# Kernel optimization log

Hardware: AMD Instinct MI355X
Metric: run time of the kernel (lower is better)

Reference implementation:

```python
import math
import jax, jax.numpy as jnp
import numpy as np

HEADS = 16


def setup_inputs() -> dict:
    key = jax.random.key(0)
    k1, k2, k3 = jax.random.split(key, 3)
    bs, n_ctx, width = 2, 2048, 1024
    x = jax.random.normal(k1, (bs, n_ctx, width), dtype=jnp.float32)
    # init_scale=0.25 style small init for stability
    W_qkv = jax.random.normal(k2, (width, 3 * width), dtype=jnp.float32) * (0.25 / math.sqrt(width))
    b_qkv = jnp.zeros((3 * width,), dtype=jnp.float32)
    W_proj = jax.random.normal(k3, (width, width), dtype=jnp.float32) * (0.25 / math.sqrt(width))
    b_proj = jnp.zeros((width,), dtype=jnp.float32)
    return {"x": x, "W_qkv": W_qkv, "b_qkv": b_qkv, "W_proj": W_proj, "b_proj": b_proj}


def reference(x, W_qkv, b_qkv, W_proj, b_proj):
    bs, n_ctx, width = x.shape
    qkv = x @ W_qkv + b_qkv                     # [b, s, 3*width]
    attn_ch = width // HEADS                    # head dim
    qkv = qkv.reshape(bs, n_ctx, HEADS, 3 * attn_ch)
    q, k, v = jnp.split(qkv, 3, axis=-1)        # each [b, s, h, c]
    scale = 1.0 / math.sqrt(math.sqrt(attn_ch)) # applied to both q and k
    weight = jnp.einsum('bthc,bshc->bhts', q * scale, k * scale)
    weight = jax.nn.softmax(weight.astype(jnp.float32), axis=-1).astype(qkv.dtype)
    out = jnp.einsum('bhts,bshc->bthc', weight, v).reshape(bs, n_ctx, width)
    return out @ W_proj + b_proj
```

## Files before the change

kernel.cpp:

```cpp
#include <hip/hip_runtime.h>


using u16 = unsigned short;
typedef __attribute__((ext_vector_type(8))) short s16x8;
typedef __attribute__((ext_vector_type(4))) float f32x4;
typedef __attribute__((ext_vector_type(16))) float f32x16;

__device__ __forceinline__ u16 f2bf(float f) {
    unsigned x = __builtin_bit_cast(unsigned, f);
    x += 0x7fffu + ((x >> 16) & 1u);
    return (u16)(x >> 16);
}
__device__ __forceinline__ float bf2f(u16 u) {
    return __builtin_bit_cast(float, ((unsigned)u) << 16);
}
__device__ __forceinline__ unsigned pk2bf(float lo, float hi) {
    unsigned a = __builtin_bit_cast(unsigned, lo);
    unsigned b = __builtin_bit_cast(unsigned, hi);
    a += 0x7fffu + ((a >> 16) & 1u);
    b += 0x7fffu + ((b >> 16) & 1u);
    return (a >> 16) | (b & 0xffff0000u);
}
__device__ __forceinline__ void gll16(const void* g, void* l) {
    __builtin_amdgcn_global_load_lds(
        (const __attribute__((address_space(1))) unsigned int*)g,
        (__attribute__((address_space(3))) unsigned int*)l, 16, 0, 0);
}

#define MFMA(a, b, c)   __builtin_amdgcn_mfma_f32_16x16x32_bf16((a), (b), (c), 0, 0, 0)
#define MFMA32(a, b, c) __builtin_amdgcn_mfma_f32_32x32x16_bf16((a), (b), (c), 0, 0, 0)


__global__ __launch_bounds__(256) void convert_split(const float* __restrict__ in,
                                                     u16* __restrict__ H, u16* __restrict__ L, int n) {
    int i = (blockIdx.x * 256 + threadIdx.x) * 4;
    if (i >= n) return;
    float4 v = *(const float4*)(in + i);
    u16 h0 = f2bf(v.x), h1 = f2bf(v.y), h2 = f2bf(v.z), h3 = f2bf(v.w);
    ushort4 hh = { h0, h1, h2, h3 };
    ushort4 ll = { f2bf(v.x - bf2f(h0)), f2bf(v.y - bf2f(h1)), f2bf(v.z - bf2f(h2)), f2bf(v.w - bf2f(h3)) };
    *(ushort4*)(H + i) = hh;
    *(ushort4*)(L + i) = ll;
}

__global__ __launch_bounds__(256) void transpose_split(const float* __restrict__ W,
                                                       u16* __restrict__ TH, u16* __restrict__ TL,
                                                       int K, int N) {
    __shared__ float st[32][33];
    int n0 = blockIdx.x * 32, k0 = blockIdx.y * 32;
    int c = threadIdx.x & 31, r8 = threadIdx.x >> 5;
#pragma unroll
    for (int i = 0; i < 4; ++i) {
        int r = r8 + i * 8;
        st[r][c] = W[(size_t)(k0 + r) * N + n0 + c];
    }
    __syncthreads();
#pragma unroll
    for (int i = 0; i < 4; ++i) {
        int r = r8 + i * 8;
        float v = st[c][r];
        u16 h = f2bf(v);
        TH[(size_t)(n0 + r) * K + k0 + c] = h;
        TL[(size_t)(n0 + r) * K + k0 + c] = f2bf(v - bf2f(h));
    }
}


template <int EPI>
__global__ __launch_bounds__(256, 2) void gemm_bf16x3(
    const u16* __restrict__ AH, const u16* __restrict__ AL,
    const u16* __restrict__ BTH, const u16* __restrict__ BTL,
    const float* __restrict__ bias,
    u16* __restrict__ Qs, u16* __restrict__ Kb, u16* __restrict__ Vp,
    float* __restrict__ Out) {
    __shared__ u16 sP[2][32][512];

    int id = blockIdx.x;
    int xcd = id & 7, local = id >> 3;
    int nPerX = gridDim.x >> 8;
    int nb = xcd * nPerX + (local >> 5);
    int mb = local & 31;
    int m0 = mb * 128, n0 = nb * 128;

    int tid = threadIdx.x, lane = tid & 63, wv = tid >> 6;
    int g = lane >> 4, c16 = lane & 15;
    int wm = wv >> 1, wn = wv & 1;
    const int lo8 = lane * 8;

    const u16* src[8];
#pragma unroll
    for (int i = 0; i < 8; ++i) {
        int p = wv * 8 + i;
        const u16* arr = (p < 8) ? AH : (p < 16) ? AL : (p < 24) ? BTH : BTL;
        int row0 = ((p < 16) ? m0 : n0) + (p & 7) * 16;
        src[i] = arr + (size_t)(row0 + c16) * 1024 + g * 8;
    }

    f32x4 acc[4][4] = {};

#pragma unroll
    for (int i = 0; i < 8; ++i) gll16(src[i], &sP[0][wv * 8 + i][0]);

    for (int kt = 0; kt < 32; ++kt) {
        int cur = kt & 1;
        __syncthreads();
        if (kt < 31) {
            int ko = (kt + 1) * 32;
#pragma unroll
            for (int i = 0; i < 8; ++i) gll16(src[i] + ko, &sP[cur ^ 1][wv * 8 + i][0]);
        }

        s16x8 ah[4], al[4], bh[4], bl[4];
#pragma unroll
        for (int mi = 0; mi < 4; ++mi) {
            ah[mi] = *(const s16x8*)&sP[cur][wm * 4 + mi][lo8];
            al[mi] = *(const s16x8*)&sP[cur][8 + wm * 4 + mi][lo8];
        }
#pragma unroll
        for (int ni = 0; ni < 4; ++ni) {
            bh[ni] = *(const s16x8*)&sP[cur][16 + wn * 4 + ni][lo8];
            bl[ni] = *(const s16x8*)&sP[cur][24 + wn * 4 + ni][lo8];
        }
#pragma unroll
        for (int mi = 0; mi < 4; ++mi)
#pragma unroll
            for (int ni = 0; ni < 4; ++ni) {
                f32x4 c = acc[mi][ni];
                c = MFMA(ah[mi], bh[ni], c);
                c = MFMA(al[mi], bh[ni], c);
                c = MFMA(ah[mi], bl[ni], c);
                acc[mi][ni] = c;
            }
    }

#pragma unroll
    for (int ni = 0; ni < 4; ++ni) {
        int col = n0 + wn * 64 + ni * 16 + c16;
        float bs = bias[col];
        if (EPI == 0) {
            int h = col / 192;
            int rm = col - h * 192;
#pragma unroll
            for (int mi = 0; mi < 4; ++mi)
#pragma unroll
                for (int r = 0; r < 4; ++r) {
                    int row = m0 + wm * 64 + mi * 16 + 4 * g + r;
                    int b = row >> 11, s = row & 2047;
                    int bh16 = b * 16 + h;
                    float val = acc[mi][ni][r] + bs;
                    if (rm < 64)
                        Qs[(((size_t)bh16 * 2048 + s) << 6) + rm] = f2bf(val * 0.18033688011112042f);
                    else if (rm < 128)
                        Kb[(((size_t)bh16 * 2048 + s) << 6) + rm - 64] = f2bf(val);
                    else {
                        int d = rm - 128;
                        int kg = s >> 4, k16 = s & 15;
                        int mm = (k16 & 3) | (((k16 >> 3) & 1) << 2) | (((k16 >> 2) & 1) << 3);
                        Vp[(((size_t)bh16 * 128 + kg) * 64 + d) * 16 + mm] = f2bf(val);
                    }
                }
        } else {
#pragma unroll
            for (int mi = 0; mi < 4; ++mi)
#pragma unroll
                for (int r = 0; r < 4; ++r) {
                    int row = m0 + wm * 64 + mi * 16 + 4 * g + r;
                    Out[(size_t)row * 1024 + col] = acc[mi][ni][r] + bs;
                }
        }
    }
}

__global__ __launch_bounds__(256, 2) void attn_fwd(
    const u16* __restrict__ Qs, const u16* __restrict__ Kb, const u16* __restrict__ Vp,
    u16* __restrict__ OH, u16* __restrict__ OL) {
    __shared__ u16 sKV[2][16][512];

    int id = blockIdx.x;
    int xcd = id & 7, li = id >> 3;
    int bh = xcd * 4 + (li >> 4);
    int qblk = li & 15;
    int tid = threadIdx.x, w = tid >> 6, lane = tid & 63;
    int l31 = lane & 31, h = lane >> 5;
    int q0 = (qblk * 4 + w) * 32;

    size_t base = (size_t)bh * 2048 * 64;
    size_t vbase = (size_t)bh * 131072;

    const u16* qp = Qs + base + (size_t)(q0 + l31) * 64 + 8 * h;
    s16x8 qf[4];
#pragma unroll
    for (int c = 0; c < 4; ++c) qf[c] = *(const s16x8*)(qp + 16 * c);

    const int pk0 = 2 * w, pk1 = 2 * w + 1;
    const u16* gk0 = Kb + base + (size_t)((pk0 >> 2) * 32 + l31) * 64 + 16 * (pk0 & 3) + 8 * h;
    const u16* gk1 = Kb + base + (size_t)((pk1 >> 2) * 32 + l31) * 64 + 16 * (pk1 & 3) + 8 * h;
    const u16* gv0 = Vp + vbase + (size_t)pk0 * 512 + (size_t)l31 * 16 + 8 * h;
    const u16* gv1 = Vp + vbase + (size_t)pk1 * 512 + (size_t)l31 * 16 + 8 * h;

    auto stage = [&](int buf, int jj) {
        size_t ko = (size_t)jj * 4096;
        gll16(gk0 + ko, &sKV[buf][pk0][0]);
        gll16(gk1 + ko, &sKV[buf][pk1][0]);
        gll16(gv0 + ko, &sKV[buf][8 + pk0][0]);
        gll16(gv1 + ko, &sKV[buf][8 + pk1][0]);
    };

    f32x16 o0 = {}, o1 = {};
    float m = -1e30f, ls = 0.f;
    const int lo = lane * 8;

    stage(0, 0);

    for (int jj = 0; jj < 32; ++jj) {
        int cur = jj & 1;
        __syncthreads();
        if (jj < 31) stage(cur ^ 1, jj + 1);

        s16x8 kf[8], vf[8];
#pragma unroll
        for (int i = 0; i < 8; ++i) {
            kf[i] = *(const s16x8*)&sKV[cur][i][lo];
            vf[i] = *(const s16x8*)&sKV[cur][8 + i][lo];
        }

        f32x16 s0 = {}, s1 = {};
        __builtin_amdgcn_s_setprio(1);
        s0 = MFMA32(kf[0], qf[0], s0);
        s0 = MFMA32(kf[1], qf[1], s0);
        s0 = MFMA32(kf[2], qf[2], s0);
        s0 = MFMA32(kf[3], qf[3], s0);
        s1 = MFMA32(kf[4], qf[0], s1);
        s1 = MFMA32(kf[5], qf[1], s1);
        s1 = MFMA32(kf[6], qf[2], s1);
        s1 = MFMA32(kf[7], qf[3], s1);
        __builtin_amdgcn_s_setprio(0);

        float t0 = fmaxf(s0[0], s1[0]), t1 = fmaxf(s0[1], s1[1]);
        float t2 = fmaxf(s0[2], s1[2]), t3 = fmaxf(s0[3], s1[3]);
#pragma unroll
        for (int r = 4; r < 16; r += 4) {
            t0 = fmaxf(t0, fmaxf(s0[r], s1[r]));
            t1 = fmaxf(t1, fmaxf(s0[r + 1], s1[r + 1]));
            t2 = fmaxf(t2, fmaxf(s0[r + 2], s1[r + 2]));
            t3 = fmaxf(t3, fmaxf(s0[r + 3], s1[r + 3]));
        }
        float pmax = fmaxf(fmaxf(t0, t1), fmaxf(t2, t3));
        pmax = fmaxf(pmax, __shfl_xor(pmax, 32));

        if (!__all(pmax <= m + 8.f)) {
            float mn = fmaxf(m, pmax);
            float f = __builtin_amdgcn_exp2f(m - mn);
            m = mn;
            ls *= f;
#pragma unroll
            for (int r = 0; r < 16; ++r) {
                float fb = __shfl(f, (r & 3) + 8 * (r >> 2) + 4 * h);
                o0[r] *= fb;
                o1[r] *= fb;
            }
        }

        float a0 = 0.f, a1 = 0.f, a2 = 0.f, a3 = 0.f;
#pragma unroll
        for (int r = 0; r < 16; r += 4) {
            s0[r]     = __builtin_amdgcn_exp2f(s0[r] - m);     a0 += s0[r];
            s0[r + 1] = __builtin_amdgcn_exp2f(s0[r + 1] - m); a1 += s0[r + 1];
            s0[r + 2] = __builtin_amdgcn_exp2f(s0[r + 2] - m); a2 += s0[r + 2];
            s0[r + 3] = __builtin_amdgcn_exp2f(s0[r + 3] - m); a3 += s0[r + 3];
            s1[r]     = __builtin_amdgcn_exp2f(s1[r] - m);     a0 += s1[r];
            s1[r + 1] = __builtin_amdgcn_exp2f(s1[r + 1] - m); a1 += s1[r + 1];
            s1[r + 2] = __builtin_amdgcn_exp2f(s1[r + 2] - m); a2 += s1[r + 2];
            s1[r + 3] = __builtin_amdgcn_exp2f(s1[r + 3] - m); a3 += s1[r + 3];
        }
        float sm = (a0 + a1) + (a2 + a3);
        sm += __shfl_xor(sm, 32);
        ls += sm;

        union { s16x8 v8; unsigned u[4]; } p00, p01, p10, p11;
#pragma unroll
        for (int k = 0; k < 4; ++k) {
            p00.u[k] = pk2bf(s0[2 * k], s0[2 * k + 1]);
            p01.u[k] = pk2bf(s0[8 + 2 * k], s0[9 + 2 * k]);
            p10.u[k] = pk2bf(s1[2 * k], s1[2 * k + 1]);
            p11.u[k] = pk2bf(s1[8 + 2 * k], s1[9 + 2 * k]);
        }

        __builtin_amdgcn_s_setprio(1);
        o0 = MFMA32(p00.v8, vf[0], o0);
        o1 = MFMA32(p00.v8, vf[1], o1);
        o0 = MFMA32(p01.v8, vf[2], o0);
        o1 = MFMA32(p01.v8, vf[3], o1);
        o0 = MFMA32(p10.v8, vf[4], o0);
        o1 = MFMA32(p10.v8, vf[5], o1);
        o0 = MFMA32(p11.v8, vf[6], o0);
        o1 = MFMA32(p11.v8, vf[7], o1);
        __builtin_amdgcn_s_setprio(0);
    }

    int b = bh >> 4, hh = bh & 15;
    float inv = 1.0f / ls;
#pragma unroll
    for (int r = 0; r < 16; ++r) {
        int cr = (r & 3) + 8 * (r >> 2) + 4 * h;
        float fb = __shfl(inv, cr);
        int row = q0 + cr;
        size_t idx = ((size_t)(b * 2048 + row)) * 1024 + hh * 64 + l31;
        float v0 = o0[r] * fb, v1 = o1[r] * fb;
        u16 h0 = f2bf(v0);
        OH[idx] = h0;
        OL[idx] = f2bf(v0 - bf2f(h0));
        u16 h1 = f2bf(v1);
        OH[idx + 32] = h1;
        OL[idx + 32] = f2bf(v1 - bf2f(h1));
    }
}


extern "C" void kernel_launch(void* const* d_in, const int* in_sizes, int n_in,
                              void* d_out, int out_size, void* d_ws, size_t ws_size,
                              hipStream_t stream) {
    const float* x     = (const float*)d_in[0];
    const float* Wqkv  = (const float*)d_in[1];
    const float* bqkv  = (const float*)d_in[2];
    const float* Wproj = (const float*)d_in[3];
    const float* bproj = (const float*)d_in[4];
    float* out = (float*)d_out;

    char* w = (char*)d_ws;
    const size_t SZ_X  = (size_t)4096 * 1024 * 2;
    const size_t SZ_WQ = (size_t)3072 * 1024 * 2;
    const size_t SZ_WP = (size_t)1024 * 1024 * 2;
    u16* XH  = (u16*)w; w += SZ_X;
    u16* XL  = (u16*)w; w += SZ_X;
    u16* WQH = (u16*)w; w += SZ_WQ;
    u16* WQL = (u16*)w; w += SZ_WQ;
    u16* WPH = (u16*)w; w += SZ_WP;
    u16* WPL = (u16*)w; w += SZ_WP;
    u16* Q_s = (u16*)w; w += SZ_X;
    u16* K_b = (u16*)w; w += SZ_X;
    u16* V_p = (u16*)w; w += SZ_X;
    u16* OHp = (u16*)w; w += SZ_X;
    u16* OLp = (u16*)w; w += SZ_X;

    convert_split<<<4096, 256, 0, stream>>>(x, XH, XL, 4096 * 1024);
    transpose_split<<<dim3(96, 32), 256, 0, stream>>>(Wqkv, WQH, WQL, 1024, 3072);
    transpose_split<<<dim3(32, 32), 256, 0, stream>>>(Wproj, WPH, WPL, 1024, 1024);
    gemm_bf16x3<0><<<768, 256, 0, stream>>>(XH, XL, WQH, WQL, bqkv, Q_s, K_b, V_p, nullptr);
    attn_fwd<<<512, 256, 0, stream>>>(Q_s, K_b, V_p, OHp, OLp);
    gemm_bf16x3<1><<<256, 256, 0, stream>>>(OHp, OLp, WPH, WPL, bproj, nullptr, nullptr, nullptr, out);
}
```

Measured before the change: 216.9 us.

## Single-buffer GEMM LDS, raise occupancy, drop XCD swizzle, add MFMA priority

```diff
diff --git a/kernel.cpp b/kernel.cpp
--- a/kernel.cpp
+++ b/kernel.cpp
@@ -67,21 +67,15 @@
 
 
 template <int EPI>
-__global__ __launch_bounds__(256, 2) void gemm_bf16x3(
+__global__ __launch_bounds__(256, 3) void gemm_bf16x3(
     const u16* __restrict__ AH, const u16* __restrict__ AL,
     const u16* __restrict__ BTH, const u16* __restrict__ BTL,
     const float* __restrict__ bias,
     u16* __restrict__ Qs, u16* __restrict__ Kb, u16* __restrict__ Vp,
     float* __restrict__ Out) {
-    __shared__ u16 sP[2][32][512];
-
-    int id = blockIdx.x;
-    int xcd = id & 7, local = id >> 3;
-    int nPerX = gridDim.x >> 8;
-    int nb = xcd * nPerX + (local >> 5);
-    int mb = local & 31;
-    int m0 = mb * 128, n0 = nb * 128;
-
+    __shared__ u16 sP[32][512];
+
+    int m0 = blockIdx.y * 128, n0 = blockIdx.x * 128;
     int tid = threadIdx.x, lane = tid & 63, wv = tid >> 6;
     int g = lane >> 4, c16 = lane & 15;
     int wm = wv >> 1, wn = wv & 1;
@@ -98,29 +92,25 @@
 
     f32x4 acc[4][4] = {};
 
-#pragma unroll
-    for (int i = 0; i < 8; ++i) gll16(src[i], &sP[0][wv * 8 + i][0]);
-
     for (int kt = 0; kt < 32; ++kt) {
-        int cur = kt & 1;
         __syncthreads();
-        if (kt < 31) {
-            int ko = (kt + 1) * 32;
-#pragma unroll
-            for (int i = 0; i < 8; ++i) gll16(src[i] + ko, &sP[cur ^ 1][wv * 8 + i][0]);
-        }
+        int ko = kt * 32;
+#pragma unroll
+        for (int i = 0; i < 8; ++i) gll16(src[i] + ko, &sP[wv * 8 + i][0]);
+        __syncthreads();
 
         s16x8 ah[4], al[4], bh[4], bl[4];
 #pragma unroll
         for (int mi = 0; mi < 4; ++mi) {
-            ah[mi] = *(const s16x8*)&sP[cur][wm * 4 + mi][lo8];
-            al[mi] = *(const s16x8*)&sP[cur][8 + wm * 4 + mi][lo8];
+            ah[mi] = *(const s16x8*)&sP[wm * 4 + mi][lo8];
+            al[mi] = *(const s16x8*)&sP[8 + wm * 4 + mi][lo8];
         }
 #pragma unroll
         for (int ni = 0; ni < 4; ++ni) {
-            bh[ni] = *(const s16x8*)&sP[cur][16 + wn * 4 + ni][lo8];
-            bl[ni] = *(const s16x8*)&sP[cur][24 + wn * 4 + ni][lo8];
-        }
+            bh[ni] = *(const s16x8*)&sP[16 + wn * 4 + ni][lo8];
+            bl[ni] = *(const s16x8*)&sP[24 + wn * 4 + ni][lo8];
+        }
+        __builtin_amdgcn_s_setprio(1);
 #pragma unroll
         for (int mi = 0; mi < 4; ++mi)
 #pragma unroll
@@ -131,6 +121,7 @@
                 c = MFMA(ah[mi], bl[ni], c);
                 acc[mi][ni] = c;
             }
+        __builtin_amdgcn_s_setprio(0);
     }
 
 #pragma unroll
@@ -346,7 +337,7 @@
     convert_split<<<4096, 256, 0, stream>>>(x, XH, XL, 4096 * 1024);
     transpose_split<<<dim3(96, 32), 256, 0, stream>>>(Wqkv, WQH, WQL, 1024, 3072);
     transpose_split<<<dim3(32, 32), 256, 0, stream>>>(Wproj, WPH, WPL, 1024, 1024);
-    gemm_bf16x3<0><<<768, 256, 0, stream>>>(XH, XL, WQH, WQL, bqkv, Q_s, K_b, V_p, nullptr);
+    gemm_bf16x3<0><<<dim3(24, 32), 256, 0, stream>>>(XH, XL, WQH, WQL, bqkv, Q_s, K_b, V_p, nullptr);
     attn_fwd<<<512, 256, 0, stream>>>(Q_s, K_b, V_p, OHp, OLp);
-    gemm_bf16x3<1><<<256, 256, 0, stream>>>(OHp, OLp, WPH, WPL, bproj, nullptr, nullptr, nullptr, out);
-}
+    gemm_bf16x3<1><<<dim3(8, 32), 256, 0, stream>>>(OHp, OLp, WPH, WPL, bproj, nullptr, nullptr, nullptr, out);
+}
```

After: 232.5 us. 1.07x slower.
